# Kernel tuning notes

Hardware: AMD Instinct MI355X
Metric: run time of the kernel (lower is better)

Reference implementation:

```python
import jax, jax.numpy as jnp
import numpy as np

B, D_IN, N, L, P, C = 512, 784, 2048, 6, 15, 10  # batch, input, width, dag layers, weight pairs, classes


def setup_inputs() -> dict:
    key = jax.random.key(0)
    ks = jax.random.split(key, 10)
    x = jax.random.normal(ks[0], (B, D_IN), jnp.float32)
    w_in = jax.random.normal(ks[1], (N, D_IN), jnp.float32) * 0.1
    b_in = jax.random.normal(ks[2], (N,), jnp.float32) * 0.1
    W = jax.random.normal(ks[3], (P, N, N), jnp.float32) * 0.1
    # binary 0/1 float masks standing in for DAG connectivity masks
    M = jax.random.bernoulli(ks[4], 0.5, (P, N, N)).astype(jnp.float32)
    b = jax.random.normal(ks[5], (L - 1, N), jnp.float32) * 0.1
    w_out1 = jax.random.normal(ks[6], (C, N), jnp.float32) * 0.1
    b_out1 = jax.random.normal(ks[7], (C,), jnp.float32) * 0.1
    w_out2 = jax.random.normal(ks[8], (C, N), jnp.float32) * 0.1
    b_out2 = jax.random.normal(ks[9], (C,), jnp.float32) * 0.1
    return {"x": x, "w_in": w_in, "b_in": b_in, "W": W, "M": M, "b": b,
            "w_out1": w_out1, "b_out1": b_out1, "w_out2": w_out2, "b_out2": b_out2}


def reference(x, w_in, b_in, W, M, b, w_out1, b_out1, w_out2, b_out2):
    # input layer
    acts = [jax.nn.relu(x @ w_in.T + b_in)]  # [B, N]
    idx = 0
    for i in range(1, L):  # DAG layer i has predecessors 0..i-1
        Wm = W[idx:idx + i] * M[idx:idx + i]          # [i, N, N] masked weights
        stacked = jnp.stack(acts)                      # [i, B, N]
        # sum over predecessors of inp @ Wm.T; bias added once per predecessor
        out = jnp.einsum('jbn,jmn->bm', stacked, Wm) + i * b[i - 1]
        acts.append(jax.nn.relu(out))
        idx += i
    return acts[-1] @ w_out1.T + b_out1 + acts[-2] @ w_out2.T + b_out2
```

## Files before the change

### kernel.cpp

```cpp
#include <hip/hip_runtime.h>

typedef __bf16 bf16;
typedef __attribute__((ext_vector_type(8))) __bf16 bf16x8;
typedef __attribute__((ext_vector_type(4))) __bf16 bf16x4;
typedef __attribute__((ext_vector_type(4))) float floatx4;

#define B_SZ 512
#define N_SZ 2048
#define DIN  784
#define DINP 800
#define ACT_LD 12288

__device__ __forceinline__ void load_lds16(const bf16* g, bf16* l) {
    __builtin_amdgcn_global_load_lds(
        (const __attribute__((address_space(1))) void*)g,
        (__attribute__((address_space(3))) void*)l, 16, 0, 0);
}

__global__ __launch_bounds__(256)
void prep_kernel(const float* __restrict__ x, const float* __restrict__ w_in,
                 bf16* __restrict__ xb, bf16* __restrict__ w_inb)
{
    int g = blockIdx.x * 256 + threadIdx.x;
    const int GPR = DINP / 4;
    const float* src; bf16* dst; int row, c;
    if (g < B_SZ * GPR) {
        row = g / GPR; c = g - row * GPR;
        src = x + (size_t)row * DIN;  dst = xb + (size_t)row * DINP;
    } else {
        int h = g - B_SZ * GPR;
        row = h / GPR; c = h - row * GPR;
        src = w_in + (size_t)row * DIN;  dst = w_inb + (size_t)row * DINP;
    }
    int k = c * 4;
    floatx4 v = (floatx4){0.f, 0.f, 0.f, 0.f};
    if (k < DIN) v = *(const floatx4*)(src + k);
    bf16x4 o;
    o[0] = (bf16)v[0]; o[1] = (bf16)v[1]; o[2] = (bf16)v[2]; o[3] = (bf16)v[3];
    *(bf16x4*)(dst + k) = o;
}

__global__ __launch_bounds__(256)
void wm_kernel(const float* __restrict__ W, const float* __restrict__ M,
               bf16* __restrict__ Wm)
{
    int g = blockIdx.x * 256 + threadIdx.x;
    int p  = g >> 20;
    int n  = (g >> 9) & 2047;
    int k4 = (g & 511) * 4;
    size_t so = ((size_t)p << 22) + ((size_t)n << 11) + k4;
    floatx4 w = *(const floatx4*)(W + so);
    floatx4 m = *(const floatx4*)(M + so);
    int i   = (p >= 10) ? 5 : (p >= 6) ? 4 : (p >= 3) ? 3 : (p >= 1) ? 2 : 1;
    int idx = i * (i - 1) / 2;
    int j   = p - idx;
    size_t dof = ((size_t)idx << 22) + (size_t)n * (N_SZ * i) + (size_t)j * N_SZ + k4;
    bf16x4 o;
    o[0] = (bf16)(w[0] * m[0]); o[1] = (bf16)(w[1] * m[1]);
    o[2] = (bf16)(w[2] * m[2]); o[3] = (bf16)(w[3] * m[3]);
    *(bf16x4*)(Wm + dof) = o;
}

__global__ __launch_bounds__(256, 2)
void gemm_kernel(const bf16* __restrict__ A, int lda,
                 const bf16* __restrict__ Bm, int ldb,
                 float* __restrict__ partial,
                 int chunkK, int Ktot)
{
    __shared__ bf16 As[128 * 32];
    __shared__ bf16 Bs[128 * 32];

    const int t    = threadIdx.x;
    const int lane = t & 63, wave = t >> 6;
    const int wm   = (wave & 1) * 64, wn = (wave >> 1) * 64;
    const int l15  = lane & 15, quad = lane >> 4;
    const int n0   = blockIdx.x * 128, m0 = blockIdx.y * 128;
    const int s    = blockIdx.z;
    const int kb   = s * chunkK;
    const int ke   = (kb + chunkK < Ktot) ? (kb + chunkK) : Ktot;

    const int rA = wave * 16 + (lane >> 2);
    const int cA = (lane & 3) * 8;
    const bf16* pA0 = A  + (size_t)(m0 + rA) * lda + cA + kb;
    const bf16* pA1 = pA0 + (size_t)64 * lda;
    const bf16* pB0 = Bm + (size_t)(n0 + rA) * ldb + cA + kb;
    const bf16* pB1 = pB0 + (size_t)64 * ldb;
    bf16* dA0 = &As[wave * 512];  bf16* dA1 = &As[(wave + 4) * 512];
    bf16* dB0 = &Bs[wave * 512];  bf16* dB1 = &Bs[(wave + 4) * 512];

    floatx4 acc[4][4];
#pragma unroll
    for (int a = 0; a < 4; a++)
#pragma unroll
        for (int b = 0; b < 4; b++) acc[a][b] = (floatx4){0.f, 0.f, 0.f, 0.f};

    for (int k0 = kb; k0 < ke; k0 += 32) {
        __syncthreads();
        load_lds16(pA0, dA0);  load_lds16(pA1, dA1);
        load_lds16(pB0, dB0);  load_lds16(pB1, dB1);
        pA0 += 32; pA1 += 32; pB0 += 32; pB1 += 32;
        __syncthreads();

        bf16x8 af[4], bfr[4];
#pragma unroll
        for (int a = 0; a < 4; a++)
            af[a] = *(const bf16x8*)(&As[(wm + a * 16 + l15) * 32 + quad * 8]);
#pragma unroll
        for (int b = 0; b < 4; b++)
            bfr[b] = *(const bf16x8*)(&Bs[(wn + b * 16 + l15) * 32 + quad * 8]);
#pragma unroll
        for (int a = 0; a < 4; a++)
#pragma unroll
            for (int b = 0; b < 4; b++)
                acc[a][b] = __builtin_amdgcn_mfma_f32_16x16x32_bf16(af[a], bfr[b], acc[a][b], 0, 0, 0);
    }

    float* outp = partial + (size_t)s * (B_SZ * N_SZ);
#pragma unroll
    for (int a = 0; a < 4; a++)
#pragma unroll
        for (int b = 0; b < 4; b++)
#pragma unroll
            for (int r = 0; r < 4; r++) {
                int row = m0 + wm + a * 16 + quad * 4 + r;
                int col = n0 + wn + b * 16 + l15;
                outp[(size_t)row * N_SZ + col] = acc[a][b][r];
            }
}

__global__ __launch_bounds__(256)
void epilogue_kernel(const float* __restrict__ partial, int S,
                     const float* __restrict__ bias, float bscale,
                     bf16* __restrict__ actdst)
{
    int g = blockIdx.x * 256 + threadIdx.x;
    size_t off = (size_t)g * 4;
    int b = (int)(off >> 11);
    int n = (int)(off & (N_SZ - 1));
    floatx4 v = *(const floatx4*)(partial + off);
    for (int s2 = 1; s2 < S; s2++)
        v += *(const floatx4*)(partial + (size_t)s2 * (B_SZ * N_SZ) + off);
    floatx4 bv = *(const floatx4*)(bias + n);
    bf16x4 o;
#pragma unroll
    for (int j = 0; j < 4; j++) {
        float xv = v[j] + bscale * bv[j];
        xv = xv > 0.f ? xv : 0.f;
        o[j] = (bf16)xv;
    }
    *(bf16x4*)(actdst + (size_t)b * ACT_LD + n) = o;
}

__global__ __launch_bounds__(64)
void out_kernel(const bf16* __restrict__ act4, const bf16* __restrict__ act5,
                const float* __restrict__ w1, const float* __restrict__ b1,
                const float* __restrict__ w2, const float* __restrict__ b2,
                float* __restrict__ out)
{
    int b = blockIdx.x, lane = threadIdx.x;
    float a5[32], a4[32];
#pragma unroll
    for (int rep = 0; rep < 4; rep++) {
        bf16x8 v5 = *(const bf16x8*)(act5 + (size_t)b * ACT_LD + rep * 512 + lane * 8);
        bf16x8 v4 = *(const bf16x8*)(act4 + (size_t)b * ACT_LD + rep * 512 + lane * 8);
#pragma unroll
        for (int j = 0; j < 8; j++) {
            a5[rep * 8 + j] = (float)v5[j];
            a4[rep * 8 + j] = (float)v4[j];
        }
    }
    for (int c = 0; c < 10; c++) {
        float d = 0.f;
#pragma unroll
        for (int rep = 0; rep < 4; rep++) {
            floatx4 wa = *(const floatx4*)(w1 + (size_t)c * N_SZ + rep * 512 + lane * 8);
            floatx4 wb = *(const floatx4*)(w1 + (size_t)c * N_SZ + rep * 512 + lane * 8 + 4);
            floatx4 va = *(const floatx4*)(w2 + (size_t)c * N_SZ + rep * 512 + lane * 8);
            floatx4 vb = *(const floatx4*)(w2 + (size_t)c * N_SZ + rep * 512 + lane * 8 + 4);
#pragma unroll
            for (int j = 0; j < 4; j++) {
                d += a5[rep * 8 + j] * wa[j] + a4[rep * 8 + j] * va[j];
                d += a5[rep * 8 + 4 + j] * wb[j] + a4[rep * 8 + 4 + j] * vb[j];
            }
        }
        for (int off = 32; off > 0; off >>= 1) d += __shfl_down(d, off);
        if (lane == 0) out[b * 10 + c] = d + b1[c] + b2[c];
    }
}

extern "C" void kernel_launch(void* const* d_in, const int* in_sizes, int n_in,
                              void* d_out, int out_size, void* d_ws, size_t ws_size,
                              hipStream_t stream)
{
    const float* x    = (const float*)d_in[0];
    const float* w_in = (const float*)d_in[1];
    const float* b_in = (const float*)d_in[2];
    const float* W    = (const float*)d_in[3];
    const float* M    = (const float*)d_in[4];
    const float* bL   = (const float*)d_in[5];
    const float* w1   = (const float*)d_in[6];
    const float* b1   = (const float*)d_in[7];
    const float* w2   = (const float*)d_in[8];
    const float* b2   = (const float*)d_in[9];
    float* out = (float*)d_out;

    char* ws = (char*)d_ws;
    bf16*  xb      = (bf16*)ws;
    bf16*  w_inb   = (bf16*)(ws + 819200);
    bf16*  actsT   = (bf16*)(ws + 4096000);
    float* partial = (float*)(ws + 16678912);
    bf16*  Wm      = (bf16*)(ws + 50233344);

    prep_kernel<<<2000, 256, 0, stream>>>(x, w_in, xb, w_inb);
    wm_kernel<<<61440, 256, 0, stream>>>(W, M, Wm);

    gemm_kernel<<<dim3(16, 4, 4), 256, 0, stream>>>(
        xb, DINP, w_inb, DINP, partial, 224, DINP);
    epilogue_kernel<<<1024, 256, 0, stream>>>(partial, 4, b_in, 1.0f, actsT);

    for (int i = 1; i < 6; i++) {
        int idx = i * (i - 1) / 2;
        const bf16* Bl = Wm + ((size_t)idx << 22);
        gemm_kernel<<<dim3(16, 4, 8), 256, 0, stream>>>(
            actsT, ACT_LD, Bl, N_SZ * i, partial, 256 * i, N_SZ * i);
        epilogue_kernel<<<1024, 256, 0, stream>>>(
            partial, 8, bL + (size_t)(i - 1) * N_SZ, (float)i,
            actsT + (size_t)i * N_SZ);
    }

    out_kernel<<<512, 64, 0, stream>>>(
        actsT + (size_t)4 * N_SZ, actsT + (size_t)5 * N_SZ,
        w1, b1, w2, b2, out);
}
```

Baseline: 715.3 us.

## Fuse weight masking and bf16 conversion into DAG GEMM B-tile loads

Removes the separate masking kernel that wrote a bf16 copy of W*M to workspace. The new DAG GEMM reads fp32 W and M directly, multiplies and converts them in registers, and stores the B tile to LDS, prefetching the next tile in registers. Tiles change to 256x64 so each W/M element is read by only two M-blocks, which cuts the redundant fp32 weight traffic. The cost is more global bytes per B element and a register-staged B path instead of direct-to-LDS loads.

```diff
diff --git a/kernel.cpp b/kernel.cpp
--- a/kernel.cpp
+++ b/kernel.cpp
@@ -40,27 +40,6 @@
     *(bf16x4*)(dst + k) = o;
 }
 
-__global__ __launch_bounds__(256)
-void wm_kernel(const float* __restrict__ W, const float* __restrict__ M,
-               bf16* __restrict__ Wm)
-{
-    int g = blockIdx.x * 256 + threadIdx.x;
-    int p  = g >> 20;
-    int n  = (g >> 9) & 2047;
-    int k4 = (g & 511) * 4;
-    size_t so = ((size_t)p << 22) + ((size_t)n << 11) + k4;
-    floatx4 w = *(const floatx4*)(W + so);
-    floatx4 m = *(const floatx4*)(M + so);
-    int i   = (p >= 10) ? 5 : (p >= 6) ? 4 : (p >= 3) ? 3 : (p >= 1) ? 2 : 1;
-    int idx = i * (i - 1) / 2;
-    int j   = p - idx;
-    size_t dof = ((size_t)idx << 22) + (size_t)n * (N_SZ * i) + (size_t)j * N_SZ + k4;
-    bf16x4 o;
-    o[0] = (bf16)(w[0] * m[0]); o[1] = (bf16)(w[1] * m[1]);
-    o[2] = (bf16)(w[2] * m[2]); o[3] = (bf16)(w[3] * m[3]);
-    *(bf16x4*)(Wm + dof) = o;
-}
-
 __global__ __launch_bounds__(256, 2)
 void gemm_kernel(const bf16* __restrict__ A, int lda,
                  const bf16* __restrict__ Bm, int ldb,
@@ -124,6 +103,100 @@
             for (int r = 0; r < 4; r++) {
                 int row = m0 + wm + a * 16 + quad * 4 + r;
                 int col = n0 + wn + b * 16 + l15;
+                outp[(size_t)row * N_SZ + col] = acc[a][b][r];
+            }
+}
+
+__global__ __launch_bounds__(256, 2)
+void dag_gemm_kernel(const bf16* __restrict__ A,
+                     const float* __restrict__ Wl, const float* __restrict__ Ml,
+                     float* __restrict__ partial,
+                     int chunkK, int Ktot)
+{
+    __shared__ bf16 As[256 * 32];
+    __shared__ bf16 Bs[64 * 32];
+
+    const int t    = threadIdx.x;
+    const int lane = t & 63, wave = t >> 6;
+    const int l15  = lane & 15, quad = lane >> 4;
+    const int n0   = blockIdx.x * 64, m0 = blockIdx.y * 256;
+    const int s    = blockIdx.z;
+    const int kb   = s * chunkK;
+    const int ke   = kb + chunkK;
+
+    const int ar = wave * 16 + (lane >> 2);
+    const int ac = (lane & 3) * 8;
+    const bf16* pA0 = A + (size_t)(m0 +   0 + ar) * ACT_LD + kb + ac;
+    const bf16* pA1 = A + (size_t)(m0 +  64 + ar) * ACT_LD + kb + ac;
+    const bf16* pA2 = A + (size_t)(m0 + 128 + ar) * ACT_LD + kb + ac;
+    const bf16* pA3 = A + (size_t)(m0 + 192 + ar) * ACT_LD + kb + ac;
+    bf16* dA0 = &As[(  0 + wave * 16) * 32];
+    bf16* dA1 = &As[( 64 + wave * 16) * 32];
+    bf16* dA2 = &As[(128 + wave * 16) * 32];
+    bf16* dA3 = &As[(192 + wave * 16) * 32];
+
+    const int br = t >> 2, bc = (t & 3) * 8;
+    const size_t wrow = (size_t)(n0 + br) << 11;
+
+    floatx4 acc[4][4];
+#pragma unroll
+    for (int a = 0; a < 4; a++)
+#pragma unroll
+        for (int b = 0; b < 4; b++) acc[a][b] = (floatx4){0.f, 0.f, 0.f, 0.f};
+
+    floatx4 wr0, wr1, mr0, mr1;
+    {
+        int jj = kb >> 11, kk = kb & 2047;
+        size_t o = ((size_t)jj << 22) + wrow + kk + bc;
+        wr0 = *(const floatx4*)(Wl + o);  wr1 = *(const floatx4*)(Wl + o + 4);
+        mr0 = *(const floatx4*)(Ml + o);  mr1 = *(const floatx4*)(Ml + o + 4);
+    }
+
+    for (int k0 = kb; k0 < ke; k0 += 32) {
+        __syncthreads();
+        load_lds16(pA0, dA0);  load_lds16(pA1, dA1);
+        load_lds16(pA2, dA2);  load_lds16(pA3, dA3);
+        pA0 += 32; pA1 += 32; pA2 += 32; pA3 += 32;
+
+        bf16x8 o8;
+        o8[0] = (bf16)(wr0[0] * mr0[0]); o8[1] = (bf16)(wr0[1] * mr0[1]);
+        o8[2] = (bf16)(wr0[2] * mr0[2]); o8[3] = (bf16)(wr0[3] * mr0[3]);
+        o8[4] = (bf16)(wr1[0] * mr1[0]); o8[5] = (bf16)(wr1[1] * mr1[1]);
+        o8[6] = (bf16)(wr1[2] * mr1[2]); o8[7] = (bf16)(wr1[3] * mr1[3]);
+        *(bf16x8*)(&Bs[br * 32 + bc]) = o8;
+
+        if (k0 + 32 < ke) {
+            int kn = k0 + 32;
+            int jj = kn >> 11, kk = kn & 2047;
+            size_t o = ((size_t)jj << 22) + wrow + kk + bc;
+            wr0 = *(const floatx4*)(Wl + o);  wr1 = *(const floatx4*)(Wl + o + 4);
+            mr0 = *(const floatx4*)(Ml + o);  mr1 = *(const floatx4*)(Ml + o + 4);
+        }
+        __syncthreads();
+
+        bf16x8 af[4], bfr[4];
+#pragma unroll
+        for (int a = 0; a < 4; a++)
+            af[a] = *(const bf16x8*)(&As[(wave * 64 + a * 16 + l15) * 32 + quad * 8]);
+#pragma unroll
+        for (int b = 0; b < 4; b++)
+            bfr[b] = *(const bf16x8*)(&Bs[(b * 16 + l15) * 32 + quad * 8]);
+#pragma unroll
+        for (int a = 0; a < 4; a++)
+#pragma unroll
+            for (int b = 0; b < 4; b++)
+                acc[a][b] = __builtin_amdgcn_mfma_f32_16x16x32_bf16(af[a], bfr[b], acc[a][b], 0, 0, 0);
+    }
+
+    float* outp = partial + (size_t)s * (B_SZ * N_SZ);
+#pragma unroll
+    for (int a = 0; a < 4; a++)
+#pragma unroll
+        for (int b = 0; b < 4; b++)
+#pragma unroll
+            for (int r = 0; r < 4; r++) {
+                int row = m0 + wave * 64 + a * 16 + quad * 4 + r;
+                int col = n0 + b * 16 + l15;
                 outp[(size_t)row * N_SZ + col] = acc[a][b][r];
             }
 }
@@ -209,10 +282,8 @@
     bf16*  w_inb   = (bf16*)(ws + 819200);
     bf16*  actsT   = (bf16*)(ws + 4096000);
     float* partial = (float*)(ws + 16678912);
-    bf16*  Wm      = (bf16*)(ws + 50233344);
 
     prep_kernel<<<2000, 256, 0, stream>>>(x, w_in, xb, w_inb);
-    wm_kernel<<<61440, 256, 0, stream>>>(W, M, Wm);
 
     gemm_kernel<<<dim3(16, 4, 4), 256, 0, stream>>>(
         xb, DINP, w_inb, DINP, partial, 224, DINP);
@@ -220,9 +291,10 @@
 
     for (int i = 1; i < 6; i++) {
         int idx = i * (i - 1) / 2;
-        const bf16* Bl = Wm + ((size_t)idx << 22);
-        gemm_kernel<<<dim3(16, 4, 8), 256, 0, stream>>>(
-            actsT, ACT_LD, Bl, N_SZ * i, partial, 256 * i, N_SZ * i);
+        const float* Wl = W + ((size_t)idx << 22);
+        const float* Ml = M + ((size_t)idx << 22);
+        dag_gemm_kernel<<<dim3(32, 2, 8), 256, 0, stream>>>(
+            actsT, Wl, Ml, partial, 256 * i, 2048 * i);
         epilogue_kernel<<<1024, 256, 0, stream>>>(
             partial, 8, bL + (size_t)(i - 1) * N_SZ, (float)i,
             actsT + (size_t)i * N_SZ);
```

Measured after the change: 714.2 us. About the same (-0.2%).
